# Performance work log

Hardware: AMD Instinct MI355X
Metric: run time of the kernel (lower is better)

Reference implementation:

```python
import jax, jax.numpy as jnp
import numpy as np

HEAD_COUNT = 16
HEAD_DIM = 128  # embed_count // head_count = 2048 // 16


def setup_inputs() -> dict:
    key = jax.random.key(0)
    k0, k1, k2, k3, k4 = jax.random.split(key, 5)
    B, C, S = 4, 2048, 1024
    keys = jax.random.normal(k0, (B, C, 1, S), dtype=jnp.float32)
    values = jax.random.normal(k1, (B, C, 1, S), dtype=jnp.float32)
    queries = jax.random.normal(k2, (B, C, 1, S), dtype=jnp.float32)
    attention_mask = jax.random.randint(k3, (B, S), 0, 2).astype(bool)
    # guarantee at least one valid key per batch row so softmax is finite
    attention_mask = attention_mask.at[:, 0].set(True)
    w_out = jax.random.normal(k4, (C, C), dtype=jnp.float32) * 0.02
    return {"keys": keys, "values": values, "queries": queries,
            "attention_mask": attention_mask, "w_out": w_out}


def reference(keys, values, queries, attention_mask, w_out):
    B, C, _, S = keys.shape
    h, d = HEAD_COUNT, HEAD_DIM
    # keys: [B,C,1,S] -> transpose(1,3) -> [B,S,1,C] -> [B,S,h,d]
    k = jnp.transpose(keys[:, :, 0, :], (0, 2, 1)).reshape(B, S, h, d)      # bkhd
    # values/queries: [B,C,1,S] -> [B,h,d,S] -> transpose(1,2) -> [B,d,h,S]
    v = jnp.transpose(values[:, :, 0, :].reshape(B, h, d, S), (0, 2, 1, 3))  # bdhk
    q = jnp.transpose(queries[:, :, 0, :].reshape(B, h, d, S), (0, 2, 1, 3)) # bdhq
    # additive mask bias: 0 where attended, -inf where masked; broadcast over h,q
    bias = jnp.where(attention_mask, 0.0, -jnp.inf).astype(keys.dtype)       # [B,K]
    scale = 1.0 / np.sqrt(d).astype(np.float32)
    w = jnp.einsum('bdhq,bkhd->bkhq', q * scale, k)                          # [B,K,h,Q]
    w = w + bias[:, :, None, None]
    w = jax.nn.softmax(w, axis=1)  # softmax over keys (dim 1)
    hid = jnp.einsum('bkhq,bdhk->bdhq', w, v)                                # [B,d,h,Q]
    hid = jnp.transpose(hid, (0, 2, 1, 3)).reshape(B, C, S)                  # [B,C,Q]
    out = jnp.einsum('oc,bcq->boq', w_out, hid)                              # 1x1 conv out_proj
    return out.reshape(B, C, 1, S)
```

## Files before the change

kernel.cpp:

```cpp
#include <hip/hip_runtime.h>

#define Bq 4
#define Cc 2048
#define Ss 1024
#define Hh 16
#define Dd 128

#define QSCALE 0.127517429f

typedef __bf16 bf16x8 __attribute__((ext_vector_type(8)));
typedef float  f32x4  __attribute__((ext_vector_type(4)));

__device__ __forceinline__ ushort f2bf(float f) {
    uint u = __float_as_uint(f);
    u += 0x7FFFu + ((u >> 16) & 1u);
    return (ushort)(u >> 16);
}
__device__ __forceinline__ uint pack2bf(float a, float b) {
    return (uint)f2bf(a) | ((uint)f2bf(b) << 16);
}
__device__ __forceinline__ void gld16(const void* g, void* l) {
    __builtin_amdgcn_global_load_lds(
        (const __attribute__((address_space(1))) unsigned int*)g,
        (__attribute__((address_space(3))) unsigned int*)l, 16, 0, 0);
}

__global__ __launch_bounds__(256) void mask_bias_k(const unsigned* __restrict__ mask,
                                                   float* __restrict__ bias) {
    __shared__ int f01, ff;
    const int t = threadIdx.x;
    if (t == 0) { f01 = 0; ff = 0; }
    __syncthreads();
    int a = 0, b = 0;
    for (int i = t; i < 1024; i += 256) {
        unsigned v = mask[i];
        if (v != 0u && v != 1u) a = 1;
        if (v != 0u && v != 0x3F800000u) b = 1;
    }
    if (a) atomicOr(&f01, 1);
    if (b) atomicOr(&ff, 1);
    __syncthreads();
    const int mode = f01 ? (ff ? 1 : 2) : 0;
    const int* mi = (const int*)mask;
    const unsigned char* mb = (const unsigned char*)mask;
    const float* mf = (const float*)mask;
    for (int i = t; i < Bq * Ss; i += 256) {
        bool on;
        if (mode == 0)      on = (mi[i] != 0);
        else if (mode == 1) on = (mb[i] != 0);
        else                on = (mf[i] != 0.0f);
        bias[i] = on ? 0.0f : -1e30f;
    }
}

__global__ __launch_bounds__(256) void wcvt_swz(const float* __restrict__ w,
                                                ushort* __restrict__ wb) {
    const size_t e = ((size_t)blockIdx.x * 256 + threadIdx.x) * 8;
    const int row = (int)(e >> 11), col = (int)(e & 2047);
    const int colS = (col & ~63) | ((col & 63) ^ ((row & 7) << 3));
    float4 v0 = *(const float4*)&w[e];
    float4 v1 = *(const float4*)&w[e + 4];
    uint4 o;
    o.x = pack2bf(v0.x, v0.y); o.y = pack2bf(v0.z, v0.w);
    o.z = pack2bf(v1.x, v1.y); o.w = pack2bf(v1.z, v1.w);
    *(uint4*)&wb[(size_t)row * 2048 + colS] = o;
}

__global__ __launch_bounds__(256) void vcvt_perm(const float* __restrict__ v,
                                                 ushort* __restrict__ vb) {
    const int tid = blockIdx.x * 256 + threadIdx.x;
    const int row = tid >> 7;
    const int cp = tid & 127;
    const int blk = (cp >> 3) * 64;
    const int j0 = cp & 7;
    const int b5 = j0 >> 2, h = j0 & 3;
    const float* src = v + (size_t)row * 1024 + blk + 32 * b5 + 4 * h;
    float4 A = *(const float4*)src;
    float4 B = *(const float4*)(src + 16);
    uint4 o;
    o.x = pack2bf(A.x, A.y); o.y = pack2bf(A.z, A.w);
    o.z = pack2bf(B.x, B.y); o.w = pack2bf(B.z, B.w);
    *(uint4*)&vb[(size_t)row * 1024 + blk + ((j0 * 8) ^ ((row & 7) << 3))] = o;
}

__global__ __launch_bounds__(256) void qk_prep(const float* __restrict__ queries,
                                               const float* __restrict__ keys,
                                               ushort* __restrict__ Qt,
                                               ushort* __restrict__ Kt) {
    __shared__ float T[128][65];
    const int t = threadIdx.x;
    const int s0 = blockIdx.x * 64;
    const int bh = blockIdx.y;
    const int isK = blockIdx.z;
    const float* src = (isK ? keys : queries) + (size_t)bh * 128 * 1024;
    const float sc = isK ? 1.0f : QSCALE;

#pragma unroll
    for (int p = 0; p < 8; ++p) {
        const int d = p * 16 + (t >> 4);
        float4 v = *(const float4*)&src[(size_t)d * 1024 + s0 + (t & 15) * 4];
        T[d][(t & 15) * 4 + 0] = v.x * sc;
        T[d][(t & 15) * 4 + 1] = v.y * sc;
        T[d][(t & 15) * 4 + 2] = v.z * sc;
        T[d][(t & 15) * 4 + 3] = v.w * sc;
    }
    __syncthreads();

    ushort* outp = isK ? Kt : Qt;
#pragma unroll
    for (int p = 0; p < 4; ++p) {
        const int k = p * 16 + (t >> 4);
        const int x = t & 15;
        uint4 o;
        o.x = pack2bf(T[x * 8 + 0][k], T[x * 8 + 1][k]);
        o.y = pack2bf(T[x * 8 + 2][k], T[x * 8 + 3][k]);
        o.z = pack2bf(T[x * 8 + 4][k], T[x * 8 + 5][k]);
        o.w = pack2bf(T[x * 8 + 6][k], T[x * 8 + 7][k]);
        const size_t rowbyte = ((size_t)bh * 1024 + s0 + k) * 256;
        const int boff = isK ? ((x * 16) ^ ((k & 7) << 4)) : (x * 16);
        *(uint4*)((char*)outp + rowbyte + boff) = o;
    }
}

__global__ __launch_bounds__(512, 2) void attn6(const ushort* __restrict__ Qt,
                                                const ushort* __restrict__ Kt,
                                                const ushort* __restrict__ Vbf,
                                                const float* __restrict__ bias,
                                                ushort* __restrict__ hidT) {
    __shared__ __align__(16) char SMEM[102400];
    float* biasS = (float*)(SMEM + 98304);

    const int t = threadIdx.x, l = t & 63, w = t >> 6;
    const int kk = l & 15, g = l >> 4;

    const int bid = blockIdx.x;
    const int vid = (bid & 7) * 32 + (bid >> 3);
    const int bh = vid >> 2, qt = vid & 3;
    const int b = bh >> 4;
    const int q0 = qt * 256;
    const size_t bhbase = (size_t)bh * 1024;

    for (int i = t; i < Ss; i += 512) biasS[i] = bias[b * Ss + i];

    bf16x8 qf[2][4];
#pragma unroll
    for (int qs = 0; qs < 2; ++qs) {
        const ushort* qrow = Qt + (bhbase + q0 + w * 32 + qs * 16 + kk) * 128;
#pragma unroll
        for (int dc = 0; dc < 4; ++dc)
            qf[qs][dc] = *(const bf16x8*)(qrow + dc * 32 + g * 8);
    }

    float lrun[2] = {0.0f, 0.0f};
    f32x4 hacc[2][8];
#pragma unroll
    for (int qs = 0; qs < 2; ++qs)
#pragma unroll
        for (int i = 0; i < 8; ++i) hacc[qs][i] = (f32x4){0.f, 0.f, 0.f, 0.f};

#define ATTN_STAGE(bufi, cki)                                                   \
    {                                                                           \
        const int k0n = (cki) * 64;                                             \
        ushort* Kd = (ushort*)SMEM + (bufi) * 8192;                             \
        ushort* Vd = (ushort*)(SMEM + 49152) + (bufi) * 8192;                   \
        _Pragma("unroll")                                                       \
        for (int ii = 0; ii < 4; ++ii) {                                        \
            const int inst = ii * 8 + w;                                        \
            if (inst < 16) {                                                    \
                gld16(Kt + (bhbase + k0n + inst * 4 + (l >> 4)) * 128 +         \
                          (l & 15) * 8,                                         \
                      Kd + inst * 512);                                         \
            } else {                                                            \
                const int i2 = inst - 16;                                       \
                gld16(Vbf + ((size_t)bh * 128 + i2 * 8 + (l >> 3)) * 1024 +     \
                          k0n + (l & 7) * 8,                                    \
                      Vd + i2 * 512);                                           \
            }                                                                   \
        }                                                                       \
    }

#define ATTN_COMPUTE(bi, ck)                                                     \
    {                                                                            \
        const int k0 = (ck) * 64;                                                \
        const ushort* KTb = (const ushort*)SMEM + (bi) * 8192;                   \
        const ushort* Vsb = (const ushort*)(SMEM + 49152) + (bi) * 8192;         \
        f32x4 sc[2][4];                                                          \
        __builtin_amdgcn_s_setprio(1);                                           \
        _Pragma("unroll")                                                        \
        for (int ns = 0; ns < 4; ++ns) {                                         \
            const f32x4 ci = *(const f32x4*)&biasS[k0 + ns * 16 + g * 4];        \
            bf16x8 kf[4];                                                        \
            const ushort* kr = KTb + (ns * 16 + kk) * 128;                       \
            _Pragma("unroll")                                                    \
            for (int dc = 0; dc < 4; ++dc)                                       \
                kf[dc] = *(const bf16x8*)(kr +                                   \
                             ((dc * 32 + g * 8) ^ ((kk & 7) << 3)));             \
            _Pragma("unroll")                                                    \
            for (int qs = 0; qs < 2; ++qs) {                                     \
                f32x4 a = ci;                                                    \
                _Pragma("unroll")                                                \
                for (int dc = 0; dc < 4; ++dc)                                   \
                    a = __builtin_amdgcn_mfma_f32_16x16x32_bf16(                 \
                        kf[dc], qf[qs][dc], a, 0, 0, 0);                         \
                sc[qs][ns] = a;                                                  \
            }                                                                    \
        }                                                                        \
        __builtin_amdgcn_s_setprio(0);                                           \
        bf16x8 pb[2][2];                                                         \
        _Pragma("unroll")                                                        \
        for (int qs = 0; qs < 2; ++qs) {                                         \
            float pv[4][4];                                                      \
            float s = 0.0f;                                                      \
            _Pragma("unroll")                                                    \
            for (int ns = 0; ns < 4; ++ns) {                                     \
                _Pragma("unroll")                                                \
                for (int r = 0; r < 4; ++r) {                                    \
                    float p = exp2f(sc[qs][ns][r]);                              \
                    pv[ns][r] = p;                                               \
                    s += p;                                                      \
                }                                                                \
            }                                                                    \
            lrun[qs] += s;                                                       \
            _Pragma("unroll")                                                    \
            for (int kh = 0; kh < 2; ++kh) {                                     \
                bf16x8 vpk;                                                      \
                _Pragma("unroll")                                                \
                for (int j = 0; j < 8; ++j)                                      \
                    vpk[j] = (__bf16)pv[2 * kh + (j >> 2)][j & 3];               \
                pb[qs][kh] = vpk;                                                \
            }                                                                    \
        }                                                                        \
        __builtin_amdgcn_s_setprio(1);                                           \
        _Pragma("unroll")                                                        \
        for (int kh = 0; kh < 2; ++kh) {                                         \
            _Pragma("unroll")                                                    \
            for (int ds = 0; ds < 8; ++ds) {                                     \
                bf16x8 vf = *(const bf16x8*)(Vsb + (ds * 16 + kk) * 64 +         \
                                 ((kh * 32 + g * 8) ^ ((kk & 7) << 3)));         \
                hacc[0][ds] = __builtin_amdgcn_mfma_f32_16x16x32_bf16(           \
                    vf, pb[0][kh], hacc[0][ds], 0, 0, 0);                        \
                hacc[1][ds] = __builtin_amdgcn_mfma_f32_16x16x32_bf16(           \
                    vf, pb[1][kh], hacc[1][ds], 0, 0, 0);                        \
            }                                                                    \
        }                                                                        \
        __builtin_amdgcn_s_setprio(0);                                           \
    }

    ATTN_STAGE(0, 0);
    ATTN_STAGE(1, 1);
    asm volatile("s_waitcnt vmcnt(4)" ::: "memory");
    __builtin_amdgcn_s_barrier();

    int cb = 0, sb = 2;
    for (int ck = 0; ck < 14; ++ck) {
        ATTN_STAGE(sb, ck + 2);
        ATTN_COMPUTE(cb, ck);
        asm volatile("s_waitcnt vmcnt(4)" ::: "memory");
        __builtin_amdgcn_s_barrier();
        cb = (cb == 2) ? 0 : cb + 1;
        sb = (sb == 2) ? 0 : sb + 1;
    }
    ATTN_COMPUTE(cb, 14);
    asm volatile("s_waitcnt vmcnt(0)" ::: "memory");
    __builtin_amdgcn_s_barrier();
    cb = (cb == 2) ? 0 : cb + 1;
    ATTN_COMPUTE(cb, 15);
#undef ATTN_STAGE
#undef ATTN_COMPUTE

    float linv[2];
#pragma unroll
    for (int qs = 0; qs < 2; ++qs) {
        float s = lrun[qs];
        s += __shfl_xor(s, 16);
        s += __shfl_xor(s, 32);
        linv[qs] = 1.0f / s;
    }

    __syncthreads();
    {
        ushort* hs = (ushort*)SMEM;
#pragma unroll
        for (int qs = 0; qs < 2; ++qs) {
            const int row = w * 32 + qs * 16 + kk;
#pragma unroll
            for (int ds = 0; ds < 8; ++ds) {
                uint2 pk;
                pk.x = pack2bf(hacc[qs][ds][0] * linv[qs], hacc[qs][ds][1] * linv[qs]);
                pk.y = pack2bf(hacc[qs][ds][2] * linv[qs], hacc[qs][ds][3] * linv[qs]);
                const int off = row * 256 + ((ds * 32 + g * 8) ^ ((row & 7) << 4));
                *(uint2*)((char*)hs + off) = pk;
            }
        }
    }
    __syncthreads();

    const int hh = bh & 15;
    const char* hsb = (const char*)SMEM;
#pragma unroll
    for (int it = 0; it < 8; ++it) {
        const int idx = it * 512 + t;
        const int q = idx >> 4, x = idx & 15;
        uint4 vv = *(const uint4*)(hsb + q * 256 + x * 16);
        *(uint4*)((char*)hidT + ((size_t)(b * Ss + q0 + q)) * 4096 + hh * 256 + x * 16) = vv;
    }
}

__global__ __launch_bounds__(512, 2) void proj4(const ushort* __restrict__ Wbf,
                                                const ushort* __restrict__ hidT,
                                                float* __restrict__ out) {
    __shared__ __align__(16) char SMEM[147456];
    const int t = threadIdx.x, l = t & 63, w = t >> 6;
    const int kk = l & 15, g = l >> 4;
    const int wr = w >> 2, wc = w & 3;

    const int bid = blockIdx.x;
    const int vid = (bid & 7) * 32 + (bid >> 3);
    const int o0 = (vid & 15) * 128;
    const int n0 = (vid >> 4) * 256;

    f32x4 acc[4][4];
#pragma unroll
    for (int i = 0; i < 4; ++i)
#pragma unroll
        for (int j = 0; j < 4; ++j) acc[i][j] = (f32x4){0.f, 0.f, 0.f, 0.f};

    const int swz = ((kk & 7) << 3);

#define P4_STAGE_A(st, ks)                                                      \
    {                                                                           \
        ushort* Ad = (ushort*)SMEM + (st) * 8192;                               \
        _Pragma("unroll")                                                       \
        for (int ii = 0; ii < 2; ++ii) {                                        \
            const int i = ii * 8 + w;                                           \
            gld16(Wbf + (size_t)(o0 + i * 8 + (l >> 3)) * 2048 + (ks) * 64 +    \
                      (l & 7) * 8,                                              \
                  Ad + i * 512);                                                \
        }                                                                       \
    }
#define P4_STAGE_B(st, ks, jj0)                                                 \
    {                                                                           \
        ushort* Bd = (ushort*)(SMEM + 49152) + (st) * 16384;                    \
        _Pragma("unroll")                                                       \
        for (int jj = (jj0); jj < (jj0) + 2; ++jj) {                            \
            const int j = jj * 8 + w;                                           \
            gld16(hidT + (size_t)(n0 + j * 8 + (l >> 3)) * 2048 + (ks) * 64 +   \
                      (l & 7) * 8,                                              \
                  Bd + j * 512);                                                \
        }                                                                       \
    }
#define P4_MFMA(nsv)                                                            \
    __builtin_amdgcn_s_setprio(1);                                              \
    _Pragma("unroll")                                                           \
    for (int dc = 0; dc < 2; ++dc)                                              \
        _Pragma("unroll")                                                       \
        for (int ms = 0; ms < 4; ++ms)                                          \
            acc[ms][nsv] = __builtin_amdgcn_mfma_f32_16x16x32_bf16(             \
                af[dc][ms], bfr[dc], acc[ms][nsv], 0, 0, 0);                    \
    __builtin_amdgcn_s_setprio(0);
#define P4_BF(nsv)                                                              \
    _Pragma("unroll")                                                           \
    for (int dc = 0; dc < 2; ++dc)                                              \
        bfr[dc] = *(const bf16x8*)&Bb[(wc * 64 + (nsv) * 16 + kk) * 64 +        \
                                      ((dc * 32 + g * 8) ^ swz)];
#define P4_BAR()  __builtin_amdgcn_s_barrier()
#define P4_LGKM() asm volatile("s_waitcnt lgkmcnt(0)" ::: "memory")

    P4_STAGE_A(0, 0); P4_STAGE_B(0, 0, 0); P4_STAGE_B(0, 0, 2);
    P4_STAGE_A(1, 1); P4_STAGE_B(1, 1, 0); P4_STAGE_B(1, 1, 2);
    asm volatile("s_waitcnt vmcnt(6)" ::: "memory");
    P4_BAR();

    int ct = 0, st = 2;
    for (int tt = 0; tt < 32; ++tt) {
        const ushort* Ab = (const ushort*)SMEM + ct * 8192;
        const ushort* Bb = (const ushort*)(SMEM + 49152) + ct * 16384;
        const int ksS = tt + 2;
        bf16x8 af[2][4], bfr[2];

#pragma unroll
        for (int dc = 0; dc < 2; ++dc)
#pragma unroll
            for (int ms = 0; ms < 4; ++ms)
                af[dc][ms] = *(const bf16x8*)&Ab[(wr * 64 + ms * 16 + kk) * 64 +
                                                 ((dc * 32 + g * 8) ^ swz)];
        P4_BF(0);
        if (tt < 30) P4_STAGE_A(st, ksS);
        P4_BAR(); P4_LGKM();
        P4_MFMA(0);
        P4_BAR();

        P4_BF(1);
        if (tt < 30) P4_STAGE_B(st, ksS, 0);
        P4_BAR(); P4_LGKM();
        P4_MFMA(1);
        P4_BAR();

        P4_BF(2);
        if (tt < 30) P4_STAGE_B(st, ksS, 2);
        P4_BAR(); P4_LGKM();
        P4_MFMA(2);
        P4_BAR();

        P4_BF(3);
        if (tt < 30)       { asm volatile("s_waitcnt vmcnt(6)" ::: "memory"); }
        else if (tt == 30) { asm volatile("s_waitcnt vmcnt(0)" ::: "memory"); }
        P4_BAR(); P4_LGKM();
        P4_MFMA(3);
        P4_BAR();

        ct = (ct == 2) ? 0 : ct + 1;
        st = (st == 2) ? 0 : st + 1;
    }
#undef P4_STAGE_A
#undef P4_STAGE_B
#undef P4_MFMA
#undef P4_BF
#undef P4_BAR
#undef P4_LGKM

#pragma unroll
    for (int ms = 0; ms < 4; ++ms)
#pragma unroll
        for (int ns = 0; ns < 4; ++ns) {
            const int o = o0 + wr * 64 + ms * 16 + g * 4;
            const int n = n0 + wc * 64 + ns * 16 + kk;
            const int bb = n >> 10, qq = n & 1023;
            float* op = out + ((size_t)(bb * Cc + o)) * Ss + qq;
#pragma unroll
            for (int r = 0; r < 4; ++r) op[(size_t)r * Ss] = acc[ms][ns][r];
        }
}

extern "C" void kernel_launch(void* const* d_in, const int* in_sizes, int n_in,
                              void* d_out, int out_size, void* d_ws, size_t ws_size,
                              hipStream_t stream) {
    const float*    keys    = (const float*)d_in[0];
    const float*    values  = (const float*)d_in[1];
    const float*    queries = (const float*)d_in[2];
    const unsigned* mask    = (const unsigned*)d_in[3];
    const float*    w_out   = (const float*)d_in[4];
    float* out = (float*)d_out;

    char* ws = (char*)d_ws;
    float*  bias = (float*)ws;
    ushort* Wbf  = (ushort*)(ws + 16384);
    ushort* Qt   = (ushort*)(ws + 16384 + (8u << 20));
    ushort* Kt   = (ushort*)(ws + 16384 + (24u << 20));
    ushort* Vbf  = (ushort*)(ws + 16384 + (40u << 20));
    ushort* hidT = (ushort*)(ws + 16384 + (56u << 20));

    hipLaunchKernelGGL(mask_bias_k, dim3(1), dim3(256), 0, stream, mask, bias);
    hipLaunchKernelGGL(wcvt_swz, dim3(2048), dim3(256), 0, stream, w_out, Wbf);
    hipLaunchKernelGGL(vcvt_perm, dim3(4096), dim3(256), 0, stream, values, Vbf);
    hipLaunchKernelGGL(qk_prep, dim3(16, 64, 2), dim3(256), 0, stream,
                       queries, keys, Qt, Kt);
    hipLaunchKernelGGL(attn6, dim3(256), dim3(512), 0, stream,
                       Qt, Kt, Vbf, bias, hidT);
    hipLaunchKernelGGL(proj4, dim3(256), dim3(512), 0, stream,
                       Wbf, hidT, out);
}
```

Measured before the change: 128.1 us.

## Merge prep kernels, fold Q conversion and mask bias into attention, restructure projection loop

```diff
diff --git a/kernel.cpp b/kernel.cpp
--- a/kernel.cpp
+++ b/kernel.cpp
@@ -25,110 +25,79 @@
         (__attribute__((address_space(3))) unsigned int*)l, 16, 0, 0);
 }
 
-__global__ __launch_bounds__(256) void mask_bias_k(const unsigned* __restrict__ mask,
-                                                   float* __restrict__ bias) {
-    __shared__ int f01, ff;
+__global__ __launch_bounds__(256) void prep_all(const float* __restrict__ w,
+                                                const float* __restrict__ v,
+                                                const float* __restrict__ keys,
+                                                ushort* __restrict__ wb,
+                                                ushort* __restrict__ vb,
+                                                ushort* __restrict__ Kt) {
+    __shared__ __align__(16) float T[128][65];
     const int t = threadIdx.x;
-    if (t == 0) { f01 = 0; ff = 0; }
-    __syncthreads();
-    int a = 0, b = 0;
-    for (int i = t; i < 1024; i += 256) {
-        unsigned v = mask[i];
-        if (v != 0u && v != 1u) a = 1;
-        if (v != 0u && v != 0x3F800000u) b = 1;
-    }
-    if (a) atomicOr(&f01, 1);
-    if (b) atomicOr(&ff, 1);
-    __syncthreads();
-    const int mode = f01 ? (ff ? 1 : 2) : 0;
-    const int* mi = (const int*)mask;
-    const unsigned char* mb = (const unsigned char*)mask;
-    const float* mf = (const float*)mask;
-    for (int i = t; i < Bq * Ss; i += 256) {
-        bool on;
-        if (mode == 0)      on = (mi[i] != 0);
-        else if (mode == 1) on = (mb[i] != 0);
-        else                on = (mf[i] != 0.0f);
-        bias[i] = on ? 0.0f : -1e30f;
-    }
-}
-
-__global__ __launch_bounds__(256) void wcvt_swz(const float* __restrict__ w,
-                                                ushort* __restrict__ wb) {
-    const size_t e = ((size_t)blockIdx.x * 256 + threadIdx.x) * 8;
-    const int row = (int)(e >> 11), col = (int)(e & 2047);
-    const int colS = (col & ~63) | ((col & 63) ^ ((row & 7) << 3));
-    float4 v0 = *(const float4*)&w[e];
-    float4 v1 = *(const float4*)&w[e + 4];
-    uint4 o;
-    o.x = pack2bf(v0.x, v0.y); o.y = pack2bf(v0.z, v0.w);
-    o.z = pack2bf(v1.x, v1.y); o.w = pack2bf(v1.z, v1.w);
-    *(uint4*)&wb[(size_t)row * 2048 + colS] = o;
-}
-
-__global__ __launch_bounds__(256) void vcvt_perm(const float* __restrict__ v,
-                                                 ushort* __restrict__ vb) {
-    const int tid = blockIdx.x * 256 + threadIdx.x;
-    const int row = tid >> 7;
-    const int cp = tid & 127;
-    const int blk = (cp >> 3) * 64;
-    const int j0 = cp & 7;
-    const int b5 = j0 >> 2, h = j0 & 3;
-    const float* src = v + (size_t)row * 1024 + blk + 32 * b5 + 4 * h;
-    float4 A = *(const float4*)src;
-    float4 B = *(const float4*)(src + 16);
-    uint4 o;
-    o.x = pack2bf(A.x, A.y); o.y = pack2bf(A.z, A.w);
-    o.z = pack2bf(B.x, B.y); o.w = pack2bf(B.z, B.w);
-    *(uint4*)&vb[(size_t)row * 1024 + blk + ((j0 * 8) ^ ((row & 7) << 3))] = o;
-}
-
-__global__ __launch_bounds__(256) void qk_prep(const float* __restrict__ queries,
-                                               const float* __restrict__ keys,
-                                               ushort* __restrict__ Qt,
-                                               ushort* __restrict__ Kt) {
-    __shared__ float T[128][65];
-    const int t = threadIdx.x;
-    const int s0 = blockIdx.x * 64;
-    const int bh = blockIdx.y;
-    const int isK = blockIdx.z;
-    const float* src = (isK ? keys : queries) + (size_t)bh * 128 * 1024;
-    const float sc = isK ? 1.0f : QSCALE;
-
-#pragma unroll
-    for (int p = 0; p < 8; ++p) {
-        const int d = p * 16 + (t >> 4);
-        float4 v = *(const float4*)&src[(size_t)d * 1024 + s0 + (t & 15) * 4];
-        T[d][(t & 15) * 4 + 0] = v.x * sc;
-        T[d][(t & 15) * 4 + 1] = v.y * sc;
-        T[d][(t & 15) * 4 + 2] = v.z * sc;
-        T[d][(t & 15) * 4 + 3] = v.w * sc;
-    }
-    __syncthreads();
-
-    ushort* outp = isK ? Kt : Qt;
-#pragma unroll
-    for (int p = 0; p < 4; ++p) {
-        const int k = p * 16 + (t >> 4);
-        const int x = t & 15;
+    const int blk = blockIdx.x;
+
+    if (blk < 2048) {
+        const size_t e = ((size_t)blk * 256 + t) * 8;
+        const int row = (int)(e >> 11), col = (int)(e & 2047);
+        const int colS = (col & ~63) | ((col & 63) ^ ((row & 7) << 3));
+        float4 v0 = *(const float4*)&w[e];
+        float4 v1 = *(const float4*)&w[e + 4];
         uint4 o;
-        o.x = pack2bf(T[x * 8 + 0][k], T[x * 8 + 1][k]);
-        o.y = pack2bf(T[x * 8 + 2][k], T[x * 8 + 3][k]);
-        o.z = pack2bf(T[x * 8 + 4][k], T[x * 8 + 5][k]);
-        o.w = pack2bf(T[x * 8 + 6][k], T[x * 8 + 7][k]);
-        const size_t rowbyte = ((size_t)bh * 1024 + s0 + k) * 256;
-        const int boff = isK ? ((x * 16) ^ ((k & 7) << 4)) : (x * 16);
-        *(uint4*)((char*)outp + rowbyte + boff) = o;
-    }
-}
-
-__global__ __launch_bounds__(512, 2) void attn6(const ushort* __restrict__ Qt,
+        o.x = pack2bf(v0.x, v0.y); o.y = pack2bf(v0.z, v0.w);
+        o.z = pack2bf(v1.x, v1.y); o.w = pack2bf(v1.z, v1.w);
+        *(uint4*)&wb[(size_t)row * 2048 + colS] = o;
+    } else if (blk < 6144) {
+        const int tid = (blk - 2048) * 256 + t;
+        const int row = tid >> 7;
+        const int cp = tid & 127;
+        const int blk64 = (cp >> 3) * 64;
+        const int j0 = cp & 7;
+        const int b5 = j0 >> 2, h = j0 & 3;
+        const float* src = v + (size_t)row * 1024 + blk64 + 32 * b5 + 4 * h;
+        float4 A = *(const float4*)src;
+        float4 B = *(const float4*)(src + 16);
+        uint4 o;
+        o.x = pack2bf(A.x, A.y); o.y = pack2bf(A.z, A.w);
+        o.z = pack2bf(B.x, B.y); o.w = pack2bf(B.z, B.w);
+        *(uint4*)&vb[(size_t)row * 1024 + blk64 + ((j0 * 8) ^ ((row & 7) << 3))] = o;
+    } else {
+        const int b2 = blk - 6144;
+        const int s0 = (b2 & 15) * 64;
+        const int bh = b2 >> 4;
+        const float* src = keys + (size_t)bh * 128 * 1024;
+#pragma unroll
+        for (int p = 0; p < 8; ++p) {
+            const int d = p * 16 + (t >> 4);
+            float4 v4 = *(const float4*)&src[(size_t)d * 1024 + s0 + (t & 15) * 4];
+            T[d][(t & 15) * 4 + 0] = v4.x;
+            T[d][(t & 15) * 4 + 1] = v4.y;
+            T[d][(t & 15) * 4 + 2] = v4.z;
+            T[d][(t & 15) * 4 + 3] = v4.w;
+        }
+        __syncthreads();
+#pragma unroll
+        for (int p = 0; p < 4; ++p) {
+            const int k = p * 16 + (t >> 4);
+            const int x = t & 15;
+            uint4 o;
+            o.x = pack2bf(T[x * 8 + 0][k], T[x * 8 + 1][k]);
+            o.y = pack2bf(T[x * 8 + 2][k], T[x * 8 + 3][k]);
+            o.z = pack2bf(T[x * 8 + 4][k], T[x * 8 + 5][k]);
+            o.w = pack2bf(T[x * 8 + 6][k], T[x * 8 + 7][k]);
+            const size_t rowbyte = ((size_t)bh * 1024 + s0 + k) * 256;
+            const int boff = (x * 16) ^ ((k & 7) << 4);
+            *(uint4*)((char*)Kt + rowbyte + boff) = o;
+        }
+    }
+}
+
+__global__ __launch_bounds__(512, 2) void attn7(const float* __restrict__ queries,
                                                 const ushort* __restrict__ Kt,
                                                 const ushort* __restrict__ Vbf,
-                                                const float* __restrict__ bias,
+                                                const unsigned* __restrict__ mask,
                                                 ushort* __restrict__ hidT) {
-    __shared__ __align__(16) char SMEM[102400];
+    __shared__ __align__(16) char SMEM[102416];
     float* biasS = (float*)(SMEM + 98304);
+    int* flg = (int*)(SMEM + 102400);
 
     const int t = threadIdx.x, l = t & 63, w = t >> 6;
     const int kk = l & 15, g = l >> 4;
@@ -136,20 +105,57 @@
     const int bid = blockIdx.x;
     const int vid = (bid & 7) * 32 + (bid >> 3);
     const int bh = vid >> 2, qt = vid & 3;
-    const int b = bh >> 4;
+    const int b = bh >> 4, hh = bh & 15;
     const int q0 = qt * 256;
     const size_t bhbase = (size_t)bh * 1024;
 
-    for (int i = t; i < Ss; i += 512) biasS[i] = bias[b * Ss + i];
-
+    if (t == 0) { flg[0] = 0; flg[1] = 0; }
+    __syncthreads();
+    {
+        int a = 0, c = 0;
+        for (int i = t; i < 1024; i += 512) {
+            unsigned vv = mask[i];
+            if (vv != 0u && vv != 1u) a = 1;
+            if (vv != 0u && vv != 0x3F800000u) c = 1;
+        }
+        if (a) atomicOr(&flg[0], 1);
+        if (c) atomicOr(&flg[1], 1);
+        __syncthreads();
+        const int mode = flg[0] ? (flg[1] ? 1 : 2) : 0;
+        const int* mi = (const int*)mask;
+        const unsigned char* mb = (const unsigned char*)mask;
+        const float* mf = (const float*)mask;
+        for (int i = t; i < 1024; i += 512) {
+            bool on;
+            if (mode == 0)      on = (mi[b * 1024 + i] != 0);
+            else if (mode == 1) on = (mb[b * 1024 + i] != 0);
+            else                on = (mf[b * 1024 + i] != 0.0f);
+            biasS[i] = on ? 0.0f : -1e30f;
+        }
+    }
+
+    const float* Qb = queries + ((size_t)(b * Cc + hh * Dd)) * Ss;
     bf16x8 qf[2][4];
 #pragma unroll
-    for (int qs = 0; qs < 2; ++qs) {
-        const ushort* qrow = Qt + (bhbase + q0 + w * 32 + qs * 16 + kk) * 128;
-#pragma unroll
-        for (int dc = 0; dc < 4; ++dc)
-            qf[qs][dc] = *(const bf16x8*)(qrow + dc * 32 + g * 8);
-    }
+    for (int qs = 0; qs < 2; ++qs)
+#pragma unroll
+        for (int dc = 0; dc < 4; ++dc) {
+            const int q = q0 + w * 32 + qs * 16 + kk;
+            float v0 = Qb[(size_t)(dc * 32 + g * 8 + 0) * Ss + q];
+            float v1 = Qb[(size_t)(dc * 32 + g * 8 + 1) * Ss + q];
+            float v2 = Qb[(size_t)(dc * 32 + g * 8 + 2) * Ss + q];
+            float v3 = Qb[(size_t)(dc * 32 + g * 8 + 3) * Ss + q];
+            float v4 = Qb[(size_t)(dc * 32 + g * 8 + 4) * Ss + q];
+            float v5 = Qb[(size_t)(dc * 32 + g * 8 + 5) * Ss + q];
+            float v6 = Qb[(size_t)(dc * 32 + g * 8 + 6) * Ss + q];
+            float v7 = Qb[(size_t)(dc * 32 + g * 8 + 7) * Ss + q];
+            uint4 u;
+            u.x = pack2bf(v0 * QSCALE, v1 * QSCALE);
+            u.y = pack2bf(v2 * QSCALE, v3 * QSCALE);
+            u.z = pack2bf(v4 * QSCALE, v5 * QSCALE);
+            u.w = pack2bf(v6 * QSCALE, v7 * QSCALE);
+            qf[qs][dc] = *(bf16x8*)&u;
+        }
 
     float lrun[2] = {0.0f, 0.0f};
     f32x4 hacc[2][8];
@@ -295,7 +301,6 @@
     }
     __syncthreads();
 
-    const int hh = bh & 15;
     const char* hsb = (const char*)SMEM;
 #pragma unroll
     for (int it = 0; it < 8; ++it) {
@@ -306,7 +311,7 @@
     }
 }
 
-__global__ __launch_bounds__(512, 2) void proj4(const ushort* __restrict__ Wbf,
+__global__ __launch_bounds__(512, 2) void proj5(const ushort* __restrict__ Wbf,
                                                 const ushort* __restrict__ hidT,
                                                 float* __restrict__ out) {
     __shared__ __align__(16) char SMEM[147456];
@@ -325,99 +330,83 @@
 #pragma unroll
         for (int j = 0; j < 4; ++j) acc[i][j] = (f32x4){0.f, 0.f, 0.f, 0.f};
 
-    const int swz = ((kk & 7) << 3);
-
-#define P4_STAGE_A(st, ks)                                                      \
+    const int swz = (kk & 7) << 3;
+
+#define P5_STAGE_A(st, ks)                                                      \
     {                                                                           \
         ushort* Ad = (ushort*)SMEM + (st) * 8192;                               \
         _Pragma("unroll")                                                       \
         for (int ii = 0; ii < 2; ++ii) {                                        \
-            const int i = ii * 8 + w;                                           \
-            gld16(Wbf + (size_t)(o0 + i * 8 + (l >> 3)) * 2048 + (ks) * 64 +    \
-                      (l & 7) * 8,                                              \
-                  Ad + i * 512);                                                \
+            const int idx = ii * 512 + t;                                       \
+            gld16(Wbf + (size_t)(o0 + (idx >> 3)) * 2048 + (ks) * 64 +          \
+                      (idx & 7) * 8,                                            \
+                  Ad + idx * 8);                                                \
         }                                                                       \
     }
-#define P4_STAGE_B(st, ks, jj0)                                                 \
+#define P5_STAGE_B(st, ks, p)                                                   \
     {                                                                           \
         ushort* Bd = (ushort*)(SMEM + 49152) + (st) * 16384;                    \
         _Pragma("unroll")                                                       \
-        for (int jj = (jj0); jj < (jj0) + 2; ++jj) {                            \
-            const int j = jj * 8 + w;                                           \
-            gld16(hidT + (size_t)(n0 + j * 8 + (l >> 3)) * 2048 + (ks) * 64 +   \
-                      (l & 7) * 8,                                              \
-                  Bd + j * 512);                                                \
+        for (int jj = (p) * 2; jj < (p) * 2 + 2; ++jj) {                        \
+            const int idx = jj * 512 + t;                                       \
+            gld16(hidT + (size_t)(n0 + (idx >> 3)) * 2048 + (ks) * 64 +         \
+                      (idx & 7) * 8,                                            \
+                  Bd + idx * 8);                                                \
         }                                                                       \
     }
-#define P4_MFMA(nsv)                                                            \
+#define P5_READ(dcv)                                                            \
+    _Pragma("unroll")                                                           \
+    for (int ms = 0; ms < 4; ++ms)                                              \
+        af[ms] = *(const bf16x8*)&Ab[(wr * 64 + ms * 16 + kk) * 64 +            \
+                                     (((dcv) * 32 + g * 8) ^ swz)];             \
+    _Pragma("unroll")                                                           \
+    for (int ns = 0; ns < 4; ++ns)                                              \
+        bfr[ns] = *(const bf16x8*)&Bb[(wc * 64 + ns * 16 + kk) * 64 +           \
+                                      (((dcv) * 32 + g * 8) ^ swz)];
+#define P5_MFMA()                                                               \
     __builtin_amdgcn_s_setprio(1);                                              \
     _Pragma("unroll")                                                           \
-    for (int dc = 0; dc < 2; ++dc)                                              \
+    for (int ms = 0; ms < 4; ++ms)                                              \
         _Pragma("unroll")                                                       \
-        for (int ms = 0; ms < 4; ++ms)                                          \
-            acc[ms][nsv] = __builtin_amdgcn_mfma_f32_16x16x32_bf16(             \
-                af[dc][ms], bfr[dc], acc[ms][nsv], 0, 0, 0);                    \
+        for (int ns = 0; ns < 4; ++ns)                                          \
+            acc[ms][ns] = __builtin_amdgcn_mfma_f32_16x16x32_bf16(              \
+                af[ms], bfr[ns], acc[ms][ns], 0, 0, 0);                         \
     __builtin_amdgcn_s_setprio(0);
-#define P4_BF(nsv)                                                              \
-    _Pragma("unroll")                                                           \
-    for (int dc = 0; dc < 2; ++dc)                                              \
-        bfr[dc] = *(const bf16x8*)&Bb[(wc * 64 + (nsv) * 16 + kk) * 64 +        \
-                                      ((dc * 32 + g * 8) ^ swz)];
-#define P4_BAR()  __builtin_amdgcn_s_barrier()
-#define P4_LGKM() asm volatile("s_waitcnt lgkmcnt(0)" ::: "memory")
-
-    P4_STAGE_A(0, 0); P4_STAGE_B(0, 0, 0); P4_STAGE_B(0, 0, 2);
-    P4_STAGE_A(1, 1); P4_STAGE_B(1, 1, 0); P4_STAGE_B(1, 1, 2);
+
+    P5_STAGE_A(0, 0); P5_STAGE_B(0, 0, 0); P5_STAGE_B(0, 0, 1);
+    P5_STAGE_A(1, 1); P5_STAGE_B(1, 1, 0); P5_STAGE_B(1, 1, 1);
     asm volatile("s_waitcnt vmcnt(6)" ::: "memory");
-    P4_BAR();
-
-    int ct = 0, st = 2;
+    __builtin_amdgcn_s_barrier();
+
+    int ct = 0, st2 = 2;
     for (int tt = 0; tt < 32; ++tt) {
         const ushort* Ab = (const ushort*)SMEM + ct * 8192;
         const ushort* Bb = (const ushort*)(SMEM + 49152) + ct * 16384;
-        const int ksS = tt + 2;
-        bf16x8 af[2][4], bfr[2];
-
-#pragma unroll
-        for (int dc = 0; dc < 2; ++dc)
-#pragma unroll
-            for (int ms = 0; ms < 4; ++ms)
-                af[dc][ms] = *(const bf16x8*)&Ab[(wr * 64 + ms * 16 + kk) * 64 +
-                                                 ((dc * 32 + g * 8) ^ swz)];
-        P4_BF(0);
-        if (tt < 30) P4_STAGE_A(st, ksS);
-        P4_BAR(); P4_LGKM();
-        P4_MFMA(0);
-        P4_BAR();
-
-        P4_BF(1);
-        if (tt < 30) P4_STAGE_B(st, ksS, 0);
-        P4_BAR(); P4_LGKM();
-        P4_MFMA(1);
-        P4_BAR();
-
-        P4_BF(2);
-        if (tt < 30) P4_STAGE_B(st, ksS, 2);
-        P4_BAR(); P4_LGKM();
-        P4_MFMA(2);
-        P4_BAR();
-
-        P4_BF(3);
-        if (tt < 30)       { asm volatile("s_waitcnt vmcnt(6)" ::: "memory"); }
-        else if (tt == 30) { asm volatile("s_waitcnt vmcnt(0)" ::: "memory"); }
-        P4_BAR(); P4_LGKM();
-        P4_MFMA(3);
-        P4_BAR();
+        bf16x8 af[4], bfr[4];
+
+        P5_READ(0);
+        if (tt < 30) { P5_STAGE_A(st2, tt + 2); P5_STAGE_B(st2, tt + 2, 0); }
+        __builtin_amdgcn_s_barrier();
+        asm volatile("s_waitcnt lgkmcnt(0)" ::: "memory");
+        P5_MFMA();
+        __builtin_amdgcn_s_barrier();
+
+        P5_READ(1);
+        if (tt < 30) P5_STAGE_B(st2, tt + 2, 1);
+        if (tt < 30) { asm volatile("s_waitcnt vmcnt(6)" ::: "memory"); }
+        else         { asm volatile("s_waitcnt vmcnt(0)" ::: "memory"); }
+        __builtin_amdgcn_s_barrier();
+        asm volatile("s_waitcnt lgkmcnt(0)" ::: "memory");
+        P5_MFMA();
+        __builtin_amdgcn_s_barrier();
 
         ct = (ct == 2) ? 0 : ct + 1;
-        st = (st == 2) ? 0 : st + 1;
-    }
-#undef P4_STAGE_A
-#undef P4_STAGE_B
-#undef P4_MFMA
-#undef P4_BF
-#undef P4_BAR
-#undef P4_LGKM
+        st2 = (st2 == 2) ? 0 : st2 + 1;
+    }
+#undef P5_STAGE_A
+#undef P5_STAGE_B
+#undef P5_READ
+#undef P5_MFMA
 
 #pragma unroll
     for (int ms = 0; ms < 4; ++ms)
@@ -443,20 +432,15 @@
     float* out = (float*)d_out;
 
     char* ws = (char*)d_ws;
-    float*  bias = (float*)ws;
-    ushort* Wbf  = (ushort*)(ws + 16384);
-    ushort* Qt   = (ushort*)(ws + 16384 + (8u << 20));
-    ushort* Kt   = (ushort*)(ws + 16384 + (24u << 20));
-    ushort* Vbf  = (ushort*)(ws + 16384 + (40u << 20));
-    ushort* hidT = (ushort*)(ws + 16384 + (56u << 20));
-
-    hipLaunchKernelGGL(mask_bias_k, dim3(1), dim3(256), 0, stream, mask, bias);
-    hipLaunchKernelGGL(wcvt_swz, dim3(2048), dim3(256), 0, stream, w_out, Wbf);
-    hipLaunchKernelGGL(vcvt_perm, dim3(4096), dim3(256), 0, stream, values, Vbf);
-    hipLaunchKernelGGL(qk_prep, dim3(16, 64, 2), dim3(256), 0, stream,
-                       queries, keys, Qt, Kt);
-    hipLaunchKernelGGL(attn6, dim3(256), dim3(512), 0, stream,
-                       Qt, Kt, Vbf, bias, hidT);
-    hipLaunchKernelGGL(proj4, dim3(256), dim3(512), 0, stream,
+    ushort* Wbf  = (ushort*)ws;
+    ushort* Kt   = (ushort*)(ws + (8u << 20));
+    ushort* Vbf  = (ushort*)(ws + (24u << 20));
+    ushort* hidT = (ushort*)(ws + (40u << 20));
+
+    hipLaunchKernelGGL(prep_all, dim3(7168), dim3(256), 0, stream,
+                       w_out, values, keys, Wbf, Vbf, Kt);
+    hipLaunchKernelGGL(attn7, dim3(256), dim3(512), 0, stream,
+                       queries, Kt, Vbf, mask, hidT);
+    hipLaunchKernelGGL(proj5, dim3(256), dim3(512), 0, stream,
                        Wbf, hidT, out);
 }
```

Measured after the change: 114.8 us. 1.12x faster.
